# Kernel optimization log

Measured on AMD Instinct MI355X. Metric: run time of the kernel, lower is better.

## Reference

```python
import jax, jax.numpy as jnp
import numpy as np

B, SQ, SK, D, DV = 16, 2048, 2048, 64, 64
DROPOUT_P = 0.1


def setup_inputs() -> dict:
    key = jax.random.key(0)
    k1, k2, k3, k4 = jax.random.split(key, 4)
    return {
        "query": jax.random.normal(k1, (B, SQ, D), dtype=jnp.float32),
        "key": jax.random.normal(k2, (B, SK, D), dtype=jnp.float32),
        "value": jax.random.normal(k3, (B, SK, DV), dtype=jnp.float32),
        "drop_mask": jax.random.uniform(k4, (B, SQ, SK), dtype=jnp.float32),
    }


def reference(query, key, value, drop_mask):
    # scaled dot-product attention with explicit score matrix, as in the module
    scale = jnp.sqrt(jnp.asarray(key.shape[-1], dtype=query.dtype))
    qk = jnp.einsum("bqd,bkd->bqk", query, key) / scale  # [B, SQ, SK]
    attn = jax.nn.softmax(qk, axis=-1)
    # dropout: keep where uniform > p, rescale by 1/(1-p)
    keep = (drop_mask > DROPOUT_P).astype(attn.dtype)
    attn = attn * keep / (1.0 - DROPOUT_P)
    return jnp.einsum("bqk,bkv->bqv", attn, value)  # [B, SQ, DV]
```

## Files before the change

### kernel.cpp

```cpp
#include <hip/hip_runtime.h>
#include <hip/hip_bf16.h>

#define B_ 16
#define SQ_ 2048
#define SK_ 2048
#define D_ 64
#define DV_ 64
#define INV_KEEP 1.1111111f

typedef float f4 __attribute__((ext_vector_type(4)));
typedef __bf16 bf16x2 __attribute__((ext_vector_type(2)));
typedef __bf16 bf16x8 __attribute__((ext_vector_type(8)));
typedef short s16x4 __attribute__((ext_vector_type(4)));
typedef unsigned int u32;
typedef unsigned int u32x2 __attribute__((ext_vector_type(2)));
typedef unsigned int u32x4 __attribute__((ext_vector_type(4)));

static __device__ __forceinline__ unsigned short bf16u(float f) {
    u32 u = __builtin_bit_cast(u32, f);
    u += 0x7fffu + ((u >> 16) & 1u);
    return (unsigned short)(u >> 16);
}
static __device__ __forceinline__ u32 pk2(float lo, float hi) {
    return (u32)bf16u(lo) | ((u32)bf16u(hi) << 16);
}
static __device__ __forceinline__ u32 pkc(float lo, float hi) {
    bf16x2 t = {(__bf16)lo, (__bf16)hi};
    return __builtin_bit_cast(u32, t);
}

static __device__ __forceinline__ void gload16(const void* g, void* l) {
    __builtin_amdgcn_global_load_lds(
        (const __attribute__((address_space(1))) unsigned int*)g,
        (__attribute__((address_space(3))) unsigned int*)l, 16, 0, 0);
}

static __device__ __forceinline__ f4 mfma16(s16x4 a, s16x4 b, f4 c) {
#if __has_builtin(__builtin_amdgcn_mfma_f32_16x16x16bf16_1k)
    return __builtin_amdgcn_mfma_f32_16x16x16bf16_1k(a, b, c, 0, 0, 0);
#else
    f4 d;
    asm("v_mfma_f32_16x16x16_bf16 %0, %1, %2, %3" : "=v"(d) : "v"(a), "v"(b), "v"(c));
    return d;
#endif
}

__global__ __launch_bounds__(256) void k_retile(const float* __restrict__ K,
                                                unsigned short* __restrict__ KbT) {
    int b = blockIdx.x >> 6, kt = blockIdx.x & 63;
    int t = threadIdx.x;
    int row = t >> 3, dc = t & 7;
    const float* src = K + ((size_t)(b * SK_ + kt * 32 + row)) * D_ + dc * 8;
    f4 a = *(const f4*)src;
    f4 b2 = *(const f4*)(src + 4);
    u32x4 w;
    w[0] = pk2(a.x, a.y); w[1] = pk2(a.z, a.w);
    w[2] = pk2(b2.x, b2.y); w[3] = pk2(b2.z, b2.w);
    *(u32x4*)(KbT + ((size_t)(b * 64 + kt)) * 2048 + (dc * 32 + row) * 8) = w;
}

__global__ __launch_bounds__(256) void v_retile(const float* __restrict__ V,
                                                unsigned short* __restrict__ VtT) {
    __shared__ float vt[32][65];
    int b = blockIdx.x >> 6, kt = blockIdx.x & 63;
    int t = threadIdx.x;
#pragma unroll
    for (int e = 0; e < 2; ++e) {
        int f = t * 2 + e;
        int row = f >> 4, c4 = (f & 15) * 4;
        *(f4*)&vt[row][c4] = *(const f4*)(V + ((size_t)(b * SK_ + kt * 32 + row)) * DV_ + c4);
    }
    __syncthreads();
    unsigned short* dst = VtT + ((size_t)(b * 64 + kt)) * 2048 + (size_t)t * 8;
    u32x4 w;
#pragma unroll
    for (int e = 0; e < 2; ++e) {
        int s = t * 2 + e;
        int kq = s >> 6, v = s & 63;
        w[e * 2 + 0] = pk2(vt[kq * 4 + 0][v], vt[kq * 4 + 1][v]);
        w[e * 2 + 1] = pk2(vt[kq * 4 + 2][v], vt[kq * 4 + 3][v]);
    }
    *(u32x4*)dst = w;
}

template <int SPLIT>
__global__ __launch_bounds__(256) void attn_main(const float* __restrict__ Q,
                                                 const unsigned short* __restrict__ KbT,
                                                 const unsigned short* __restrict__ VtT,
                                                 const float* __restrict__ mask,
                                                 float* __restrict__ out,
                                                 float* __restrict__ accP,
                                                 float* __restrict__ lP) {
    constexpr int NT32 = SK_ / SPLIT / 32;
    constexpr int NB = 512 * SPLIT;
    __shared__ unsigned short sK[2][2048];
    __shared__ unsigned short sV[2][2048];
    __shared__ float sM[2][2048];

    int bswz = (blockIdx.x & 7) * (NB / 8) + (blockIdx.x >> 3);
    int wid  = threadIdx.x >> 6;
    int split = bswz & (SPLIT - 1);
    int strip = (bswz / SPLIT) * 4 + wid;
    int b  = strip >> 7;
    int q0 = (strip & 127) << 4;
    int kb = split * (SK_ / SPLIT);
    int lane = threadIdx.x & 63;
    int g = lane >> 4, c = lane & 15;

    const size_t tile0 = ((size_t)b * 64 + split * NT32) * 2048;
    const unsigned short* ksrc = KbT + tile0 + (size_t)threadIdx.x * 8;
    const unsigned short* vsrc = VtT + tile0 + (size_t)threadIdx.x * 8;
    const float* msrc = mask + ((size_t)(b * SQ_ + q0 + (lane & 15))) * SK_ + kb + (lane >> 4) * 4;

    gload16(ksrc, &sK[0][wid * 512]);
    gload16(vsrc, &sV[0][wid * 512]);
    gload16(msrc,      &sM[0][wid * 512]);
    gload16(msrc + 16, &sM[0][wid * 512 + 256]);

    bf16x8 qf[2];
    {
        const float* qp = Q + ((size_t)(b * SQ_ + q0 + c)) * D_ + 8 * g;
#pragma unroll
        for (int h = 0; h < 2; ++h) {
            f4 a  = *(const f4*)(qp + h * 32);
            f4 bq = *(const f4*)(qp + h * 32 + 4);
            u32x4 wq;
            wq[0] = pk2(a.x * 0.125f, a.y * 0.125f);
            wq[1] = pk2(a.z * 0.125f, a.w * 0.125f);
            wq[2] = pk2(bq.x * 0.125f, bq.y * 0.125f);
            wq[3] = pk2(bq.z * 0.125f, bq.w * 0.125f);
            qf[h] = __builtin_bit_cast(bf16x8, wq);
        }
    }

    const unsigned short* kbL = &sK[0][0] + g * 256 + c * 8;
    const unsigned short* vbL = &sV[0][0] + g * 256 + c * 4;
    const float* mbL = &sM[0][0] + wid * 512 + (g * 16 + c) * 4;

    f4 acc[4];
#pragma unroll
    for (int vb = 0; vb < 4; ++vb) acc[vb] = (f4){0.f, 0.f, 0.f, 0.f};
    float lsum[2][4];
#pragma unroll
    for (int t = 0; t < 2; ++t)
#pragma unroll
        for (int r = 0; r < 4; ++r) lsum[t][r] = 0.f;

#pragma unroll
    for (int kt = 0; kt < NT32; ++kt) {
        const int cur = kt & 1;
        if (kt + 1 < NT32) {
            gload16(ksrc + (size_t)(kt + 1) * 2048, &sK[cur ^ 1][wid * 512]);
            gload16(vsrc + (size_t)(kt + 1) * 2048, &sV[cur ^ 1][wid * 512]);
            gload16(msrc + (kt + 1) * 32,      &sM[cur ^ 1][wid * 512]);
            gload16(msrc + (kt + 1) * 32 + 16, &sM[cur ^ 1][wid * 512 + 256]);
            asm volatile("s_waitcnt vmcnt(4)" ::: "memory");
        } else {
            asm volatile("s_waitcnt vmcnt(0)" ::: "memory");
        }
        __builtin_amdgcn_s_barrier();
        asm volatile("" ::: "memory");

        const unsigned short* kB = kbL + cur * 2048;
        const unsigned short* vB = vbL + cur * 2048;
        const float* mB = mbL + cur * 2048;
        f4 mk0 = *(const f4*)(mB);
        f4 mk1 = *(const f4*)(mB + 256);

        f4 st[2];
#pragma unroll
        for (int t = 0; t < 2; ++t) {
            u32x4 k0 = *(const u32x4*)(kB + t * 128);
            u32x4 k1 = *(const u32x4*)(kB + 1024 + t * 128);
            st[t] = (f4){0.f, 0.f, 0.f, 0.f};
            st[t] = __builtin_amdgcn_mfma_f32_16x16x32_bf16(
                __builtin_bit_cast(bf16x8, k0), qf[0], st[t], 0, 0, 0);
            st[t] = __builtin_amdgcn_mfma_f32_16x16x32_bf16(
                __builtin_bit_cast(bf16x8, k1), qf[1], st[t], 0, 0, 0);
        }
        float pd[2][4];
#pragma unroll
        for (int t = 0; t < 2; ++t) {
            const f4 mk = t ? mk1 : mk0;
#pragma unroll
            for (int r = 0; r < 4; ++r) {
                float p = __expf(st[t][r]);
                lsum[t][r] += p;
                pd[t][r] = (mk[r] > 0.1f) ? p : 0.f;
            }
        }
#pragma unroll
        for (int t = 0; t < 2; ++t) {
            u32x2 pw;
            pw[0] = pkc(pd[t][0], pd[t][1]);
            pw[1] = pkc(pd[t][2], pd[t][3]);
            s16x4 pb = __builtin_bit_cast(s16x4, pw);
#pragma unroll
            for (int vb = 0; vb < 4; ++vb) {
                u32x2 vv = *(const u32x2*)(vB + t * 1024 + vb * 64);
                acc[vb] = mfma16(__builtin_bit_cast(s16x4, vv), pb, acc[vb]);
            }
        }

        asm volatile("" ::: "memory");
        __builtin_amdgcn_s_barrier();
        asm volatile("" ::: "memory");
    }

    float lf = 0.f;
#pragma unroll
    for (int t = 0; t < 2; ++t)
#pragma unroll
        for (int r = 0; r < 4; ++r) lf += lsum[t][r];
    lf += __shfl_xor(lf, 16);
    lf += __shfl_xor(lf, 32);

    if constexpr (SPLIT == 1) {
        float li = INV_KEEP / lf;
        float* op = out + ((size_t)(b * SQ_ + q0 + c)) * DV_;
#pragma unroll
        for (int vb = 0; vb < 4; ++vb) {
            f4 o = acc[vb] * li;
            __builtin_nontemporal_store(o, (f4*)(op + 16 * vb + 4 * g));
        }
    } else {
        float* ap = accP + (((size_t)strip * SPLIT + split) * 64 + lane) * 16;
#pragma unroll
        for (int vb = 0; vb < 4; ++vb)
            *(f4*)(ap + 4 * vb) = acc[vb];
        if (g == 0)
            lP[((size_t)strip * SPLIT + split) * 16 + c] = lf;
    }
}

__global__ __launch_bounds__(256) void attn_combine(const float* __restrict__ accP,
                                                    const float* __restrict__ lP,
                                                    float* __restrict__ out) {
    __shared__ float sacc[4 * 1280];
    __shared__ float sl[64];
    int strip = blockIdx.x;
    int t = threadIdx.x;
    const float* src = accP + (size_t)strip * 4096;
#pragma unroll
    for (int s = 0; s < 4; ++s)
        *(f4*)&sacc[s * 1280 + (t >> 2) * 20 + (t & 3) * 4] = *(const f4*)(src + s * 1024 + t * 4);
    if (t < 64) sl[t] = lP[(size_t)strip * 64 + t];
    __syncthreads();

    int q = t >> 4, j = t & 15;
    float L = sl[q] + sl[16 + q] + sl[32 + q] + sl[48 + q];
    float inv = INV_KEEP / L;
    int base = (16 * (j & 3) + q) * 20 + 4 * (j >> 2);
    f4 o = (f4){0.f, 0.f, 0.f, 0.f};
#pragma unroll
    for (int s = 0; s < 4; ++s)
        o += *(const f4*)&sacc[s * 1280 + base];
    o *= inv;
    int b  = strip >> 7;
    int q0 = (strip & 127) << 4;
    __builtin_nontemporal_store(o, (f4*)(out + ((size_t)(b * SQ_ + q0 + q)) * DV_ + 4 * j));
}

extern "C" void kernel_launch(void* const* d_in, const int* in_sizes, int n_in,
                              void* d_out, int out_size, void* d_ws, size_t ws_size,
                              hipStream_t stream) {
    const float* Q = (const float*)d_in[0];
    const float* K = (const float*)d_in[1];
    const float* V = (const float*)d_in[2];
    const float* M = (const float*)d_in[3];
    float* out = (float*)d_out;

    char* ws = (char*)d_ws;
    unsigned short* KbT  = (unsigned short*)ws;
    unsigned short* VtT  = (unsigned short*)(ws + (size_t)4 * 1024 * 1024);
    float*          accP = (float*)         (ws + (size_t)8 * 1024 * 1024);
    float*          lP   = (float*)         (ws + (size_t)40 * 1024 * 1024);

    const size_t need_split = (size_t)40 * 1024 * 1024 + (size_t)2048 * 4 * 16 * 4;

    k_retile<<<1024, 256, 0, stream>>>(K, KbT);
    v_retile<<<1024, 256, 0, stream>>>(V, VtT);
    if (ws_size >= need_split) {
        attn_main<4><<<2048, 256, 0, stream>>>(Q, KbT, VtT, M, out, accP, lP);
        attn_combine<<<2048, 256, 0, stream>>>(accP, lP, out);
    } else {
        attn_main<1><<<512, 256, 0, stream>>>(Q, KbT, VtT, M, out, nullptr, nullptr);
    }
}
```

Measured before the change: 98.19 us.

## Load mask into registers, deepen K/V pipeline to 4 stages, split-K 2

The dropout mask is now loaded straight into registers with global_load_dwordx4 instead of being staged through LDS. K/V go through a 4-deep LDS ring with three tiles in flight. K and V retile layouts are changed so each lane reads contiguous 16-byte fragments. The split-K factor drops from 4 to 2, which halves the partial-accumulator traffic and the combine work but launches fewer blocks. The goal is to hide the latency of streaming the large mask and to cut LDS traffic, at the cost of more registers and lower parallelism.

```diff
diff --git a/kernel.cpp b/kernel.cpp
--- a/kernel.cpp
+++ b/kernel.cpp
@@ -33,6 +33,16 @@
     __builtin_amdgcn_global_load_lds(
         (const __attribute__((address_space(1))) unsigned int*)g,
         (__attribute__((address_space(3))) unsigned int*)l, 16, 0, 0);
+}
+
+template <int OFF>
+static __device__ __forceinline__ f4 gload_f4(const float* p) {
+    f4 d;
+    if constexpr (OFF == 0)
+        asm volatile("global_load_dwordx4 %0, %1, off" : "=v"(d) : "v"(p));
+    else
+        asm volatile("global_load_dwordx4 %0, %1, off offset:%2" : "=v"(d) : "v"(p), "i"(OFF));
+    return d;
 }
 
 static __device__ __forceinline__ f4 mfma16(s16x4 a, s16x4 b, f4 c) {
@@ -48,39 +58,38 @@
 __global__ __launch_bounds__(256) void k_retile(const float* __restrict__ K,
                                                 unsigned short* __restrict__ KbT) {
     int b = blockIdx.x >> 6, kt = blockIdx.x & 63;
-    int t = threadIdx.x;
-    int row = t >> 3, dc = t & 7;
-    const float* src = K + ((size_t)(b * SK_ + kt * 32 + row)) * D_ + dc * 8;
+    int p = threadIdx.x;
+    int s = p >> 6, g = (p >> 4) & 3, c = p & 15;
+    int t = s & 1, h = s >> 1;
+    const float* src = K + ((size_t)(b * SK_ + kt * 32 + 16 * t + c)) * D_ + 32 * h + 8 * g;
     f4 a = *(const f4*)src;
     f4 b2 = *(const f4*)(src + 4);
     u32x4 w;
     w[0] = pk2(a.x, a.y); w[1] = pk2(a.z, a.w);
     w[2] = pk2(b2.x, b2.y); w[3] = pk2(b2.z, b2.w);
-    *(u32x4*)(KbT + ((size_t)(b * 64 + kt)) * 2048 + (dc * 32 + row) * 8) = w;
+    *(u32x4*)(KbT + ((size_t)(b * 64 + kt)) * 2048 + (size_t)p * 8) = w;
 }
 
 __global__ __launch_bounds__(256) void v_retile(const float* __restrict__ V,
                                                 unsigned short* __restrict__ VtT) {
     __shared__ float vt[32][65];
     int b = blockIdx.x >> 6, kt = blockIdx.x & 63;
-    int t = threadIdx.x;
+    int tid = threadIdx.x;
 #pragma unroll
     for (int e = 0; e < 2; ++e) {
-        int f = t * 2 + e;
+        int f = tid * 2 + e;
         int row = f >> 4, c4 = (f & 15) * 4;
         *(f4*)&vt[row][c4] = *(const f4*)(V + ((size_t)(b * SK_ + kt * 32 + row)) * DV_ + c4);
     }
     __syncthreads();
-    unsigned short* dst = VtT + ((size_t)(b * 64 + kt)) * 2048 + (size_t)t * 8;
+    int vb = tid >> 6, g = (tid >> 4) & 3, c = tid & 15;
+    int v = vb * 16 + c;
     u32x4 w;
-#pragma unroll
-    for (int e = 0; e < 2; ++e) {
-        int s = t * 2 + e;
-        int kq = s >> 6, v = s & 63;
-        w[e * 2 + 0] = pk2(vt[kq * 4 + 0][v], vt[kq * 4 + 1][v]);
-        w[e * 2 + 1] = pk2(vt[kq * 4 + 2][v], vt[kq * 4 + 3][v]);
-    }
-    *(u32x4*)dst = w;
+    w[0] = pk2(vt[4 * g + 0][v], vt[4 * g + 1][v]);
+    w[1] = pk2(vt[4 * g + 2][v], vt[4 * g + 3][v]);
+    w[2] = pk2(vt[16 + 4 * g + 0][v], vt[16 + 4 * g + 1][v]);
+    w[3] = pk2(vt[16 + 4 * g + 2][v], vt[16 + 4 * g + 3][v]);
+    *(u32x4*)(VtT + ((size_t)(b * 64 + kt)) * 2048 + (size_t)tid * 8) = w;
 }
 
 template <int SPLIT>
@@ -93,9 +102,8 @@
                                                  float* __restrict__ lP) {
     constexpr int NT32 = SK_ / SPLIT / 32;
     constexpr int NB = 512 * SPLIT;
-    __shared__ unsigned short sK[2][2048];
-    __shared__ unsigned short sV[2][2048];
-    __shared__ float sM[2][2048];
+    __shared__ unsigned short sK[4][2048];
+    __shared__ unsigned short sV[4][2048];
 
     int bswz = (blockIdx.x & 7) * (NB / 8) + (blockIdx.x >> 3);
     int wid  = threadIdx.x >> 6;
@@ -110,12 +118,7 @@
     const size_t tile0 = ((size_t)b * 64 + split * NT32) * 2048;
     const unsigned short* ksrc = KbT + tile0 + (size_t)threadIdx.x * 8;
     const unsigned short* vsrc = VtT + tile0 + (size_t)threadIdx.x * 8;
-    const float* msrc = mask + ((size_t)(b * SQ_ + q0 + (lane & 15))) * SK_ + kb + (lane >> 4) * 4;
-
-    gload16(ksrc, &sK[0][wid * 512]);
-    gload16(vsrc, &sV[0][wid * 512]);
-    gload16(msrc,      &sM[0][wid * 512]);
-    gload16(msrc + 16, &sM[0][wid * 512 + 256]);
+    const float* msrc = mask + ((size_t)(b * SQ_ + q0 + c)) * SK_ + kb + 4 * g;
 
     bf16x8 qf[2];
     {
@@ -133,85 +136,81 @@
         }
     }
 
-    const unsigned short* kbL = &sK[0][0] + g * 256 + c * 8;
-    const unsigned short* vbL = &sV[0][0] + g * 256 + c * 4;
-    const float* mbL = &sM[0][0] + wid * 512 + (g * 16 + c) * 4;
+    f4 mreg[4][2];
+
+    auto stage = [&](int dst, int srct) {
+        gload16(ksrc + (size_t)srct * 2048, &sK[dst][wid * 512]);
+        gload16(vsrc + (size_t)srct * 2048, &sV[dst][wid * 512]);
+        const float* mp = msrc + (size_t)srct * 32;
+        mreg[dst][0] = gload_f4<0>(mp);
+        mreg[dst][1] = gload_f4<64>(mp);
+    };
+
+    stage(0, 0);
+    stage(1, 1);
+    stage(2, 2);
 
     f4 acc[4];
 #pragma unroll
     for (int vb = 0; vb < 4; ++vb) acc[vb] = (f4){0.f, 0.f, 0.f, 0.f};
-    float lsum[2][4];
-#pragma unroll
-    for (int t = 0; t < 2; ++t)
-#pragma unroll
-        for (int r = 0; r < 4; ++r) lsum[t][r] = 0.f;
-
-#pragma unroll
+    f4 ls0 = (f4){0.f, 0.f, 0.f, 0.f}, ls1 = (f4){0.f, 0.f, 0.f, 0.f};
+
+    const unsigned short* kbL = &sK[0][0] + lane * 8;
+    const unsigned short* vbL = &sV[0][0] + lane * 8;
+
+#pragma unroll 4
     for (int kt = 0; kt < NT32; ++kt) {
-        const int cur = kt & 1;
-        if (kt + 1 < NT32) {
-            gload16(ksrc + (size_t)(kt + 1) * 2048, &sK[cur ^ 1][wid * 512]);
-            gload16(vsrc + (size_t)(kt + 1) * 2048, &sV[cur ^ 1][wid * 512]);
-            gload16(msrc + (kt + 1) * 32,      &sM[cur ^ 1][wid * 512]);
-            gload16(msrc + (kt + 1) * 32 + 16, &sM[cur ^ 1][wid * 512 + 256]);
-            asm volatile("s_waitcnt vmcnt(4)" ::: "memory");
-        } else {
-            asm volatile("s_waitcnt vmcnt(0)" ::: "memory");
-        }
+        asm volatile("s_waitcnt vmcnt(8)" ::: "memory");
         __builtin_amdgcn_s_barrier();
-        asm volatile("" ::: "memory");
-
-        const unsigned short* kB = kbL + cur * 2048;
-        const unsigned short* vB = vbL + cur * 2048;
-        const float* mB = mbL + cur * 2048;
-        f4 mk0 = *(const f4*)(mB);
-        f4 mk1 = *(const f4*)(mB + 256);
-
-        f4 st[2];
-#pragma unroll
-        for (int t = 0; t < 2; ++t) {
-            u32x4 k0 = *(const u32x4*)(kB + t * 128);
-            u32x4 k1 = *(const u32x4*)(kB + 1024 + t * 128);
-            st[t] = (f4){0.f, 0.f, 0.f, 0.f};
-            st[t] = __builtin_amdgcn_mfma_f32_16x16x32_bf16(
-                __builtin_bit_cast(bf16x8, k0), qf[0], st[t], 0, 0, 0);
-            st[t] = __builtin_amdgcn_mfma_f32_16x16x32_bf16(
-                __builtin_bit_cast(bf16x8, k1), qf[1], st[t], 0, 0, 0);
-        }
-        float pd[2][4];
-#pragma unroll
-        for (int t = 0; t < 2; ++t) {
-            const f4 mk = t ? mk1 : mk0;
-#pragma unroll
-            for (int r = 0; r < 4; ++r) {
-                float p = __expf(st[t][r]);
-                lsum[t][r] += p;
-                pd[t][r] = (mk[r] > 0.1f) ? p : 0.f;
-            }
-        }
-#pragma unroll
-        for (int t = 0; t < 2; ++t) {
-            u32x2 pw;
-            pw[0] = pkc(pd[t][0], pd[t][1]);
-            pw[1] = pkc(pd[t][2], pd[t][3]);
-            s16x4 pb = __builtin_bit_cast(s16x4, pw);
-#pragma unroll
-            for (int vb = 0; vb < 4; ++vb) {
-                u32x2 vv = *(const u32x2*)(vB + t * 1024 + vb * 64);
-                acc[vb] = mfma16(__builtin_bit_cast(s16x4, vv), pb, acc[vb]);
-            }
-        }
-
-        asm volatile("" ::: "memory");
+        __builtin_amdgcn_sched_barrier(0);
+
+        const int bi = kt & 3;
+        const unsigned short* kB = kbL + bi * 2048;
+        const unsigned short* vB = vbL + bi * 2048;
+
+        u32x4 ka0 = *(const u32x4*)(kB);
+        u32x4 ka1 = *(const u32x4*)(kB + 1024);
+        u32x4 kc0 = *(const u32x4*)(kB + 512);
+        u32x4 kc1 = *(const u32x4*)(kB + 1536);
+        f4 st0 = (f4){0.f, 0.f, 0.f, 0.f}, st1 = (f4){0.f, 0.f, 0.f, 0.f};
+        st0 = __builtin_amdgcn_mfma_f32_16x16x32_bf16(__builtin_bit_cast(bf16x8, ka0), qf[0], st0, 0, 0, 0);
+        st0 = __builtin_amdgcn_mfma_f32_16x16x32_bf16(__builtin_bit_cast(bf16x8, ka1), qf[1], st0, 0, 0, 0);
+        st1 = __builtin_amdgcn_mfma_f32_16x16x32_bf16(__builtin_bit_cast(bf16x8, kc0), qf[0], st1, 0, 0, 0);
+        st1 = __builtin_amdgcn_mfma_f32_16x16x32_bf16(__builtin_bit_cast(bf16x8, kc1), qf[1], st1, 0, 0, 0);
+
+        const f4 mk0 = mreg[bi][0], mk1 = mreg[bi][1];
+        float pd0[4], pd1[4];
+#pragma unroll
+        for (int r = 0; r < 4; ++r) {
+            float p0 = __expf(st0[r]);
+            ls0[r] += p0;
+            pd0[r] = (mk0[r] > 0.1f) ? p0 : 0.f;
+            float p1 = __expf(st1[r]);
+            ls1[r] += p1;
+            pd1[r] = (mk1[r] > 0.1f) ? p1 : 0.f;
+        }
+
+        u32x2 pw0, pw1;
+        pw0[0] = pkc(pd0[0], pd0[1]); pw0[1] = pkc(pd0[2], pd0[3]);
+        pw1[0] = pkc(pd1[0], pd1[1]); pw1[1] = pkc(pd1[2], pd1[3]);
+        s16x4 pb0 = __builtin_bit_cast(s16x4, pw0);
+        s16x4 pb1 = __builtin_bit_cast(s16x4, pw1);
+#pragma unroll
+        for (int vb = 0; vb < 4; ++vb) {
+            u32x4 vv = *(const u32x4*)(vB + vb * 512);
+            u32x2 vlo, vhi;
+            vlo[0] = vv[0]; vlo[1] = vv[1];
+            vhi[0] = vv[2]; vhi[1] = vv[3];
+            acc[vb] = mfma16(__builtin_bit_cast(s16x4, vlo), pb0, acc[vb]);
+            acc[vb] = mfma16(__builtin_bit_cast(s16x4, vhi), pb1, acc[vb]);
+        }
+
         __builtin_amdgcn_s_barrier();
-        asm volatile("" ::: "memory");
-    }
-
-    float lf = 0.f;
-#pragma unroll
-    for (int t = 0; t < 2; ++t)
-#pragma unroll
-        for (int r = 0; r < 4; ++r) lf += lsum[t][r];
+        stage((kt + 3) & 3, (kt + 3 < NT32) ? (kt + 3) : (NT32 - 1));
+    }
+    asm volatile("s_waitcnt vmcnt(0)" ::: "memory");
+
+    float lf = ls0[0] + ls0[1] + ls0[2] + ls0[3] + ls1[0] + ls1[1] + ls1[2] + ls1[3];
     lf += __shfl_xor(lf, 16);
     lf += __shfl_xor(lf, 32);
 
@@ -233,28 +232,25 @@
     }
 }
 
-__global__ __launch_bounds__(256) void attn_combine(const float* __restrict__ accP,
-                                                    const float* __restrict__ lP,
-                                                    float* __restrict__ out) {
-    __shared__ float sacc[4 * 1280];
-    __shared__ float sl[64];
+__global__ __launch_bounds__(256) void attn_combine2(const float* __restrict__ accP,
+                                                     const float* __restrict__ lP,
+                                                     float* __restrict__ out) {
+    __shared__ float sacc[2 * 1280];
+    __shared__ float sl[32];
     int strip = blockIdx.x;
     int t = threadIdx.x;
-    const float* src = accP + (size_t)strip * 4096;
-#pragma unroll
-    for (int s = 0; s < 4; ++s)
+    const float* src = accP + (size_t)strip * 2048;
+#pragma unroll
+    for (int s = 0; s < 2; ++s)
         *(f4*)&sacc[s * 1280 + (t >> 2) * 20 + (t & 3) * 4] = *(const f4*)(src + s * 1024 + t * 4);
-    if (t < 64) sl[t] = lP[(size_t)strip * 64 + t];
+    if (t < 32) sl[t] = lP[(size_t)strip * 32 + t];
     __syncthreads();
 
     int q = t >> 4, j = t & 15;
-    float L = sl[q] + sl[16 + q] + sl[32 + q] + sl[48 + q];
+    float L = sl[q] + sl[16 + q];
     float inv = INV_KEEP / L;
     int base = (16 * (j & 3) + q) * 20 + 4 * (j >> 2);
-    f4 o = (f4){0.f, 0.f, 0.f, 0.f};
-#pragma unroll
-    for (int s = 0; s < 4; ++s)
-        o += *(const f4*)&sacc[s * 1280 + base];
+    f4 o = *(const f4*)&sacc[base] + *(const f4*)&sacc[1280 + base];
     o *= inv;
     int b  = strip >> 7;
     int q0 = (strip & 127) << 4;
@@ -274,15 +270,15 @@
     unsigned short* KbT  = (unsigned short*)ws;
     unsigned short* VtT  = (unsigned short*)(ws + (size_t)4 * 1024 * 1024);
     float*          accP = (float*)         (ws + (size_t)8 * 1024 * 1024);
-    float*          lP   = (float*)         (ws + (size_t)40 * 1024 * 1024);
-
-    const size_t need_split = (size_t)40 * 1024 * 1024 + (size_t)2048 * 4 * 16 * 4;
+    float*          lP   = (float*)         (ws + (size_t)24 * 1024 * 1024);
+
+    const size_t need_split = (size_t)24 * 1024 * 1024 + (size_t)2048 * 2 * 16 * 4;
 
     k_retile<<<1024, 256, 0, stream>>>(K, KbT);
     v_retile<<<1024, 256, 0, stream>>>(V, VtT);
     if (ws_size >= need_split) {
-        attn_main<4><<<2048, 256, 0, stream>>>(Q, KbT, VtT, M, out, accP, lP);
-        attn_combine<<<2048, 256, 0, stream>>>(accP, lP, out);
+        attn_main<2><<<1024, 256, 0, stream>>>(Q, KbT, VtT, M, out, accP, lP);
+        attn_combine2<<<2048, 256, 0, stream>>>(accP, lP, out);
     } else {
         attn_main<1><<<512, 256, 0, stream>>>(Q, KbT, VtT, M, out, nullptr, nullptr);
     }
```

After: 95.56 us. 2.7% less time.
